# Kernel tuning notes

Hardware: AMD Instinct MI355X
Metric: run time of the kernel (lower is better)

The kernel has to match this reference:

```python
import jax, jax.numpy as jnp
import numpy as np


def setup_inputs() -> dict:
    key = jax.random.key(0)
    k1, k2 = jax.random.split(key)
    x = jax.random.normal(k1, (4, 2048, 2048), dtype=jnp.float32)
    weight = jax.random.normal(k2, (8192, 2048), dtype=jnp.float32) * 0.02
    return {"x": x, "weight": weight, "bits": 8}


def reference(x, weight, bits):
    # ---- activation quantization (per-row int8-style) ----
    scale = jnp.clip(jnp.max(jnp.abs(x), axis=-1, keepdims=True), 1e-5)  # [..., 1]
    max_val = (1 << (bits - 1)) - 1  # 127 for 8 bits
    x_q = jnp.clip(jnp.round(x * (max_val / scale)), -max_val, max_val)

    # ---- ternary weight quantization (-1, 0, 1) ----
    w_scale = jnp.mean(jnp.abs(weight))
    w_q = jnp.where(weight > 0.5 * w_scale, 1.0, 0.0) + jnp.where(
        weight < -0.5 * w_scale, -1.0, 0.0
    )

    # ---- dequantized linear: (x_q @ (w_q * w_scale)^T) / x_scale ----
    out = jnp.einsum("bsi,oi->bso", x_q, w_q * w_scale) / scale

    # ---- squared ReLU ----
    return jnp.maximum(out, 0.0) ** 2
```

## Files before the change

### kernel.cpp

```cpp
#include <hip/hip_runtime.h>
#include <hip/hip_bf16.h>

typedef __attribute__((ext_vector_type(4))) int i32x4;

#define M_DIM 8192
#define N_DIM 8192
#define K_DIM 2048
#define WCOUNT (N_DIM * K_DIM)

__global__ __launch_bounds__(256) void k_abs_partial(const float* __restrict__ w,
                                                     float* __restrict__ part) {
    int tid = blockIdx.x * 256 + threadIdx.x;
    const float4* w4 = (const float4*)w;
    float s = 0.0f;
    const int total4 = WCOUNT / 4;
    for (int i = tid; i < total4; i += 2048 * 256) {
        float4 v = w4[i];
        s += fabsf(v.x) + fabsf(v.y) + fabsf(v.z) + fabsf(v.w);
    }
    #pragma unroll
    for (int off = 1; off < 64; off <<= 1) s += __shfl_xor(s, off);
    __shared__ float red[4];
    if ((threadIdx.x & 63) == 0) red[threadIdx.x >> 6] = s;
    __syncthreads();
    if (threadIdx.x == 0)
        part[blockIdx.x] = (red[0] + red[1]) + (red[2] + red[3]);
}

__global__ __launch_bounds__(256) void k_abs_final(const float* __restrict__ part,
                                                   float* __restrict__ sum) {
    int t = threadIdx.x;
    float s = 0.0f;
    #pragma unroll
    for (int i = 0; i < 8; i++) s += part[t + i * 256];
    #pragma unroll
    for (int off = 1; off < 64; off <<= 1) s += __shfl_xor(s, off);
    __shared__ float red[4];
    if ((t & 63) == 0) red[t >> 6] = s;
    __syncthreads();
    if (t == 0) sum[0] = (red[0] + red[1]) + (red[2] + red[3]);
}

__global__ __launch_bounds__(256) void k_wquant(const float* __restrict__ w,
                                                const float* __restrict__ sum,
                                                unsigned int* __restrict__ wq) {
    const float thr = 0.5f * (sum[0] * (1.0f / 16777216.0f));
    int tid = blockIdx.x * 256 + threadIdx.x;
    const float4* w4 = (const float4*)w;
    const int total4 = WCOUNT / 4;
    for (int i = tid; i < total4; i += 2048 * 256) {
        float4 v = w4[i];
        union { signed char c[4]; unsigned int u; } q;
        q.c[0] = v.x > thr ? 1 : (v.x < -thr ? -1 : 0);
        q.c[1] = v.y > thr ? 1 : (v.y < -thr ? -1 : 0);
        q.c[2] = v.z > thr ? 1 : (v.z < -thr ? -1 : 0);
        q.c[3] = v.w > thr ? 1 : (v.w < -thr ? -1 : 0);
        wq[i] = q.u;
    }
}

__global__ __launch_bounds__(256) void k_xquant(const float* __restrict__ x,
                                                signed char* __restrict__ xq,
                                                float* __restrict__ scale) {
    const int row = blockIdx.x;
    const int t = threadIdx.x;
    const float4* xr = (const float4*)(x + (size_t)row * K_DIM);
    float4 a = xr[t * 2];
    float4 b = xr[t * 2 + 1];
    float m = fmaxf(fmaxf(fmaxf(fabsf(a.x), fabsf(a.y)), fmaxf(fabsf(a.z), fabsf(a.w))),
                    fmaxf(fmaxf(fabsf(b.x), fabsf(b.y)), fmaxf(fabsf(b.z), fabsf(b.w))));
    #pragma unroll
    for (int off = 1; off < 64; off <<= 1) m = fmaxf(m, __shfl_xor(m, off));
    __shared__ float red[4];
    if ((t & 63) == 0) red[t >> 6] = m;
    __syncthreads();
    m = fmaxf(fmaxf(red[0], red[1]), fmaxf(red[2], red[3]));
    const float sc = fmaxf(m, 1e-5f);
    if (t == 0) scale[row] = sc;
    const float r = 127.0f / sc;
    float q[8] = {a.x, a.y, a.z, a.w, b.x, b.y, b.z, b.w};
    union { signed char c[8]; uint2 v; } pk;
    #pragma unroll
    for (int j = 0; j < 8; j++) {
        float v = rintf(q[j] * r);
        v = fminf(fmaxf(v, -127.0f), 127.0f);
        pk.c[j] = (signed char)v;
    }
    *(uint2*)(xq + (size_t)row * K_DIM + t * 8) = pk.v;
}

#define GLDS16(g, l)                                                                   \
    __builtin_amdgcn_global_load_lds((const __attribute__((address_space(1))) void*)(g), \
                                     (__attribute__((address_space(3))) void*)(l), 16, 0, 0)

__global__ __launch_bounds__(256) void k_gemm(const signed char* __restrict__ Aq,
                                              const signed char* __restrict__ Bq,
                                              const float* __restrict__ scale,
                                              const float* __restrict__ sum,
                                              float* __restrict__ out) {
    __shared__ signed char As[128 * 64];
    __shared__ signed char Bs[128 * 64];

    const int t = threadIdx.x;
    const int lane = t & 63;
    const int wid = t >> 6;
    const int wr = wid >> 1;
    const int wc = wid & 1;
    const int brow = blockIdx.y;
    const int bcol = blockIdx.x;

    const int c0 = t, c1 = t + 256;
    const int g0 = ((c0 & 3) ^ ((c0 >> 3) & 3)) * 16;
    const int g1 = ((c1 & 3) ^ ((c1 >> 3) & 3)) * 16;
    const signed char* ga0 = Aq + (size_t)(brow * 128 + (c0 >> 2)) * K_DIM + g0;
    const signed char* ga1 = Aq + (size_t)(brow * 128 + (c1 >> 2)) * K_DIM + g1;
    const signed char* gb0 = Bq + (size_t)(bcol * 128 + (c0 >> 2)) * K_DIM + g0;
    const signed char* gb1 = Bq + (size_t)(bcol * 128 + (c1 >> 2)) * K_DIM + g1;
    signed char* lA0 = As + wid * 1024;
    signed char* lA1 = As + 4096 + wid * 1024;
    signed char* lB0 = Bs + wid * 1024;
    signed char* lB1 = Bs + 4096 + wid * 1024;

    i32x4 zero = {0, 0, 0, 0};
    i32x4 acc[4][4];
    #pragma unroll
    for (int m = 0; m < 4; m++)
        #pragma unroll
        for (int n = 0; n < 4; n++) acc[m][n] = zero;

    const int swz = ((lane >> 4) ^ ((lane >> 1) & 3)) * 16;
    const int a_off = (wr * 64 + (lane & 15)) * 64 + swz;
    const int b_off = (wc * 64 + (lane & 15)) * 64 + swz;

    for (int kt = 0; kt < K_DIM; kt += 64) {
        GLDS16(ga0, lA0);
        GLDS16(ga1, lA1);
        GLDS16(gb0, lB0);
        GLDS16(gb1, lB1);
        ga0 += 64; ga1 += 64; gb0 += 64; gb1 += 64;
        __syncthreads();

        i32x4 af[4], bfr[4];
        #pragma unroll
        for (int m = 0; m < 4; m++) af[m] = *(const i32x4*)&As[a_off + m * 1024];
        #pragma unroll
        for (int n = 0; n < 4; n++) bfr[n] = *(const i32x4*)&Bs[b_off + n * 1024];
        #pragma unroll
        for (int m = 0; m < 4; m++)
            #pragma unroll
            for (int n = 0; n < 4; n++)
                acc[m][n] = __builtin_amdgcn_mfma_i32_16x16x64_i8(af[m], bfr[n], acc[m][n], 0, 0, 0);
        __syncthreads();
    }

    const float wsc = sum[0] * (1.0f / 16777216.0f);
    const int rbase = brow * 128 + wr * 64 + ((lane >> 4) * 4);
    const int cbase = bcol * 128 + wc * 64 + (lane & 15);
    #pragma unroll
    for (int m = 0; m < 4; m++) {
        #pragma unroll
        for (int j = 0; j < 4; j++) {
            const int grow = rbase + m * 16 + j;
            const float coef = wsc / scale[grow];
            #pragma unroll
            for (int n = 0; n < 4; n++) {
                float v = (float)acc[m][n][j] * coef;
                v = fmaxf(v, 0.0f);
                out[(size_t)grow * N_DIM + cbase + n * 16] = v * v;
            }
        }
    }
}

extern "C" void kernel_launch(void* const* d_in, const int* in_sizes, int n_in,
                              void* d_out, int out_size, void* d_ws, size_t ws_size,
                              hipStream_t stream) {
    const float* x = (const float*)d_in[0];
    const float* w = (const float*)d_in[1];
    float* out = (float*)d_out;

    char* ws = (char*)d_ws;
    float* sum   = (float*)ws;
    float* part  = (float*)(ws + 256);
    float* scale = (float*)(ws + 16384);
    signed char* xq = (signed char*)(ws + 65536);
    signed char* wq = (signed char*)(ws + 65536 + 16777216);

    k_abs_partial<<<2048, 256, 0, stream>>>(w, part);
    k_abs_final<<<1, 256, 0, stream>>>(part, sum);
    k_wquant<<<2048, 256, 0, stream>>>(w, sum, (unsigned int*)wq);
    k_xquant<<<M_DIM, 256, 0, stream>>>(x, xq, scale);
    k_gemm<<<dim3(N_DIM / 128, M_DIM / 128), 256, 0, stream>>>(xq, wq, scale, sum, out);
}
```

Measured before the change: 223.7 us.

## Rewrite int8 GEMM with 256x256 tiles, double-buffered LDS and staged prefetch

```diff
diff --git a/kernel.cpp b/kernel.cpp
--- a/kernel.cpp
+++ b/kernel.cpp
@@ -6,6 +6,7 @@
 #define M_DIM 8192
 #define N_DIM 8192
 #define K_DIM 2048
+#define BK 128
 #define WCOUNT (N_DIM * K_DIM)
 
 __global__ __launch_bounds__(256) void k_abs_partial(const float* __restrict__ w,
@@ -93,83 +94,138 @@
     __builtin_amdgcn_global_load_lds((const __attribute__((address_space(1))) void*)(g), \
                                      (__attribute__((address_space(3))) void*)(l), 16, 0, 0)
 
-__global__ __launch_bounds__(256) void k_gemm(const signed char* __restrict__ Aq,
-                                              const signed char* __restrict__ Bq,
-                                              const float* __restrict__ scale,
-                                              const float* __restrict__ sum,
-                                              float* __restrict__ out) {
-    __shared__ signed char As[128 * 64];
-    __shared__ signed char Bs[128 * 64];
+#define AOFF(b, h) ((b) * 32768 + (h) * 16384)
+#define BOFF(b, h) (65536 + (b) * 32768 + (h) * 16384)
+#define BAR __builtin_amdgcn_s_barrier()
+#define VMCNT4 do { asm volatile("s_waitcnt vmcnt(4)" ::: "memory"); __builtin_amdgcn_sched_barrier(0); } while (0)
+#define VMCNT0 do { asm volatile("s_waitcnt vmcnt(0)" ::: "memory"); __builtin_amdgcn_sched_barrier(0); } while (0)
+
+__global__ __launch_bounds__(512, 2) void k_gemm(const signed char* __restrict__ Aq,
+                                                 const signed char* __restrict__ Bq,
+                                                 const float* __restrict__ scale,
+                                                 const float* __restrict__ sum,
+                                                 float* __restrict__ out) {
+    __shared__ signed char lds[131072];
 
     const int t = threadIdx.x;
     const int lane = t & 63;
     const int wid = t >> 6;
-    const int wr = wid >> 1;
-    const int wc = wid & 1;
-    const int brow = blockIdx.y;
-    const int bcol = blockIdx.x;
-
-    const int c0 = t, c1 = t + 256;
-    const int g0 = ((c0 & 3) ^ ((c0 >> 3) & 3)) * 16;
-    const int g1 = ((c1 & 3) ^ ((c1 >> 3) & 3)) * 16;
-    const signed char* ga0 = Aq + (size_t)(brow * 128 + (c0 >> 2)) * K_DIM + g0;
-    const signed char* ga1 = Aq + (size_t)(brow * 128 + (c1 >> 2)) * K_DIM + g1;
-    const signed char* gb0 = Bq + (size_t)(bcol * 128 + (c0 >> 2)) * K_DIM + g0;
-    const signed char* gb1 = Bq + (size_t)(bcol * 128 + (c1 >> 2)) * K_DIM + g1;
-    signed char* lA0 = As + wid * 1024;
-    signed char* lA1 = As + 4096 + wid * 1024;
-    signed char* lB0 = Bs + wid * 1024;
-    signed char* lB1 = Bs + 4096 + wid * 1024;
-
-    i32x4 zero = {0, 0, 0, 0};
-    i32x4 acc[4][4];
-    #pragma unroll
-    for (int m = 0; m < 4; m++)
+    const int wm = wid >> 2;
+    const int wn = wid & 3;
+    const int lane4 = lane & 15;
+    const int hi = lane >> 4;
+
+    const int bid = blockIdx.x;
+    const int swzb = ((bid & 7) << 7) | (bid >> 3);
+    const int brow = swzb >> 5;
+    const int bcol = swzb & 31;
+
+    const int r0 = t >> 3;
+    const int r1 = 64 + r0;
+    const int g0 = ((t & 7) ^ ((t >> 4) & 7)) << 4;
+    const int g1 = (((t + 512) & 7) ^ (((t + 512) >> 4) & 7)) << 4;
+    const int sa0 = r0 * K_DIM + g0;
+    const int sa1 = r1 * K_DIM + g1;
+    const int dst0 = wid * 1024;
+    const int dst1 = wid * 1024 + 8192;
+
+    const signed char* Abase = Aq + (size_t)(brow * 256) * K_DIM;
+    const signed char* Bbase = Bq + (size_t)(bcol * 256) * K_DIM;
+
+#define STG(gb, ldsoff, half, kt) do {                                                  \
+        GLDS16((gb) + (half) * (128 * K_DIM) + (kt) * BK + sa0, lds + (ldsoff) + dst0); \
+        GLDS16((gb) + (half) * (128 * K_DIM) + (kt) * BK + sa1, lds + (ldsoff) + dst1); \
+    } while (0)
+
+    const int swz0 = (hi ^ (lane4 >> 1)) << 4;
+    const int swz1 = ((4 + hi) ^ (lane4 >> 1)) << 4;
+    const int aB0 = AOFF(0, wm) + lane4 * 128;
+    const int aB1 = AOFF(1, wm) + lane4 * 128;
+    const int bB0 = BOFF(0, wn >> 1) + ((wn & 1) * 64 + lane4) * 128;
+    const int bB1 = BOFF(1, wn >> 1) + ((wn & 1) * 64 + lane4) * 128;
+
+    i32x4 acc[8][4];
+    #pragma unroll
+    for (int m = 0; m < 8; m++)
         #pragma unroll
-        for (int n = 0; n < 4; n++) acc[m][n] = zero;
-
-    const int swz = ((lane >> 4) ^ ((lane >> 1) & 3)) * 16;
-    const int a_off = (wr * 64 + (lane & 15)) * 64 + swz;
-    const int b_off = (wc * 64 + (lane & 15)) * 64 + swz;
-
-    for (int kt = 0; kt < K_DIM; kt += 64) {
-        GLDS16(ga0, lA0);
-        GLDS16(ga1, lA1);
-        GLDS16(gb0, lB0);
-        GLDS16(gb1, lB1);
-        ga0 += 64; ga1 += 64; gb0 += 64; gb1 += 64;
-        __syncthreads();
-
-        i32x4 af[4], bfr[4];
-        #pragma unroll
-        for (int m = 0; m < 4; m++) af[m] = *(const i32x4*)&As[a_off + m * 1024];
-        #pragma unroll
-        for (int n = 0; n < 4; n++) bfr[n] = *(const i32x4*)&Bs[b_off + n * 1024];
-        #pragma unroll
-        for (int m = 0; m < 4; m++)
-            #pragma unroll
-            for (int n = 0; n < 4; n++)
-                acc[m][n] = __builtin_amdgcn_mfma_i32_16x16x64_i8(af[m], bfr[n], acc[m][n], 0, 0, 0);
-        __syncthreads();
+        for (int n = 0; n < 4; n++) acc[m][n] = (i32x4){0, 0, 0, 0};
+    i32x4 fa0[8], fa1[8], fb0[4], fb1[4];
+
+#define RDA(base, mlo) do { _Pragma("unroll") for (int m_ = 0; m_ < 4; m_++) {          \
+        fa0[(mlo) + m_] = *(const i32x4*)&lds[(base) + ((mlo) + m_) * 2048 + swz0];     \
+        fa1[(mlo) + m_] = *(const i32x4*)&lds[(base) + ((mlo) + m_) * 2048 + swz1]; } } while (0)
+#define RDB(base, nlo) do { _Pragma("unroll") for (int n_ = 0; n_ < 2; n_++) {          \
+        fb0[(nlo) + n_] = *(const i32x4*)&lds[(base) + ((nlo) + n_) * 2048 + swz0];     \
+        fb1[(nlo) + n_] = *(const i32x4*)&lds[(base) + ((nlo) + n_) * 2048 + swz1]; } } while (0)
+#define MM(mlo, nlo) do { __builtin_amdgcn_s_setprio(1);                                \
+        _Pragma("unroll") for (int m_ = 0; m_ < 4; m_++)                                \
+        _Pragma("unroll") for (int n_ = 0; n_ < 2; n_++) {                              \
+            acc[(mlo) + m_][(nlo) + n_] = __builtin_amdgcn_mfma_i32_16x16x64_i8(        \
+                fa0[(mlo) + m_], fb0[(nlo) + n_], acc[(mlo) + m_][(nlo) + n_], 0, 0, 0);\
+            acc[(mlo) + m_][(nlo) + n_] = __builtin_amdgcn_mfma_i32_16x16x64_i8(        \
+                fa1[(mlo) + m_], fb1[(nlo) + n_], acc[(mlo) + m_][(nlo) + n_], 0, 0, 0);\
+        } __builtin_amdgcn_s_setprio(0); } while (0)
+
+    STG(Abase, AOFF(0, 0), 0, 0); STG(Abase, AOFF(0, 1), 1, 0);
+    STG(Bbase, BOFF(0, 0), 0, 0); STG(Bbase, BOFF(0, 1), 1, 0);
+    STG(Abase, AOFF(1, 0), 0, 1); STG(Abase, AOFF(1, 1), 1, 1);
+    STG(Bbase, BOFF(1, 0), 0, 1); STG(Bbase, BOFF(1, 1), 1, 1);
+    asm volatile("s_waitcnt vmcnt(8)" ::: "memory");
+    __builtin_amdgcn_sched_barrier(0);
+    BAR;
+
+    #pragma unroll 1
+    for (int i = 0; i < 8; i++) {
+        const int kt = 2 * i;
+        if (i >= 1) { STG(Bbase, BOFF(1, 0), 0, kt + 1); STG(Bbase, BOFF(1, 1), 1, kt + 1); }
+        RDA(aB0, 0); RDB(bB0, 0);
+        MM(0, 0);
+        BAR;
+        RDA(aB0, 4); RDB(bB0, 2);
+        MM(0, 2);
+        BAR;
+        MM(4, 0);
+        BAR;
+        if (i <= 6) { STG(Abase, AOFF(0, 0), 0, kt + 2); STG(Abase, AOFF(0, 1), 1, kt + 2); }
+        MM(4, 2);
+        if (i <= 6) VMCNT4; else VMCNT0;
+        BAR;
+        if (i <= 6) { STG(Bbase, BOFF(0, 0), 0, kt + 2); STG(Bbase, BOFF(0, 1), 1, kt + 2); }
+        RDA(aB1, 0); RDB(bB1, 0);
+        MM(0, 0);
+        BAR;
+        RDA(aB1, 4); RDB(bB1, 2);
+        MM(0, 2);
+        BAR;
+        MM(4, 0);
+        BAR;
+        if (i <= 6) { STG(Abase, AOFF(1, 0), 0, kt + 3); STG(Abase, AOFF(1, 1), 1, kt + 3); }
+        MM(4, 2);
+        if (i <= 6) VMCNT4; else VMCNT0;
+        BAR;
     }
 
     const float wsc = sum[0] * (1.0f / 16777216.0f);
-    const int rbase = brow * 128 + wr * 64 + ((lane >> 4) * 4);
-    const int cbase = bcol * 128 + wc * 64 + (lane & 15);
-    #pragma unroll
-    for (int m = 0; m < 4; m++) {
+    const int rb = brow * 256 + wm * 128 + hi * 4;
+    const int cb = bcol * 256 + wn * 64 + lane4;
+    #pragma unroll
+    for (int m = 0; m < 8; m++) {
         #pragma unroll
         for (int j = 0; j < 4; j++) {
-            const int grow = rbase + m * 16 + j;
+            const int grow = rb + m * 16 + j;
             const float coef = wsc / scale[grow];
             #pragma unroll
             for (int n = 0; n < 4; n++) {
                 float v = (float)acc[m][n][j] * coef;
                 v = fmaxf(v, 0.0f);
-                out[(size_t)grow * N_DIM + cbase + n * 16] = v * v;
+                out[(size_t)grow * N_DIM + cb + n * 16] = v * v;
             }
         }
     }
+#undef STG
+#undef RDA
+#undef RDB
+#undef MM
 }
 
 extern "C" void kernel_launch(void* const* d_in, const int* in_sizes, int n_in,
@@ -190,5 +246,5 @@
     k_abs_final<<<1, 256, 0, stream>>>(part, sum);
     k_wquant<<<2048, 256, 0, stream>>>(w, sum, (unsigned int*)wq);
     k_xquant<<<M_DIM, 256, 0, stream>>>(x, xq, scale);
-    k_gemm<<<dim3(N_DIM / 128, M_DIM / 128), 256, 0, stream>>>(xq, wq, scale, sum, out);
-}
+    k_gemm<<<dim3(1024), 512, 0, stream>>>(xq, wq, scale, sum, out);
+}
```

Result: faster. 202.0 us (-9.7%).

## Rewrite int8 GEMM with 256x256 tiles, 4-stage async LDS pipeline and XCD mapping

Applied to the files above, without the earlier changes.

```diff
diff --git a/kernel.cpp b/kernel.cpp
--- a/kernel.cpp
+++ b/kernel.cpp
@@ -93,83 +93,126 @@
     __builtin_amdgcn_global_load_lds((const __attribute__((address_space(1))) void*)(g), \
                                      (__attribute__((address_space(3))) void*)(l), 16, 0, 0)
 
-__global__ __launch_bounds__(256) void k_gemm(const signed char* __restrict__ Aq,
-                                              const signed char* __restrict__ Bq,
-                                              const float* __restrict__ scale,
-                                              const float* __restrict__ sum,
-                                              float* __restrict__ out) {
-    __shared__ signed char As[128 * 64];
-    __shared__ signed char Bs[128 * 64];
+#define BAR __builtin_amdgcn_s_barrier()
+#define LGKM6 do { asm volatile("s_waitcnt lgkmcnt(6)" ::: "memory"); __builtin_amdgcn_sched_barrier(0); } while (0)
+#define LGKM0 do { asm volatile("s_waitcnt lgkmcnt(0)" ::: "memory"); __builtin_amdgcn_sched_barrier(0); } while (0)
+#define VMCNT4 do { asm volatile("s_waitcnt vmcnt(4)" ::: "memory"); __builtin_amdgcn_sched_barrier(0); } while (0)
+#define VMCNT0 do { asm volatile("s_waitcnt vmcnt(0)" ::: "memory"); __builtin_amdgcn_sched_barrier(0); } while (0)
+
+__global__ __launch_bounds__(512, 2) void k_gemm(const signed char* __restrict__ Aq,
+                                                 const signed char* __restrict__ Bq,
+                                                 const float* __restrict__ scale,
+                                                 const float* __restrict__ sum,
+                                                 float* __restrict__ out) {
+    __shared__ signed char smem[131072];
 
     const int t = threadIdx.x;
     const int lane = t & 63;
     const int wid = t >> 6;
-    const int wr = wid >> 1;
-    const int wc = wid & 1;
-    const int brow = blockIdx.y;
-    const int bcol = blockIdx.x;
-
-    const int c0 = t, c1 = t + 256;
-    const int g0 = ((c0 & 3) ^ ((c0 >> 3) & 3)) * 16;
-    const int g1 = ((c1 & 3) ^ ((c1 >> 3) & 3)) * 16;
-    const signed char* ga0 = Aq + (size_t)(brow * 128 + (c0 >> 2)) * K_DIM + g0;
-    const signed char* ga1 = Aq + (size_t)(brow * 128 + (c1 >> 2)) * K_DIM + g1;
-    const signed char* gb0 = Bq + (size_t)(bcol * 128 + (c0 >> 2)) * K_DIM + g0;
-    const signed char* gb1 = Bq + (size_t)(bcol * 128 + (c1 >> 2)) * K_DIM + g1;
-    signed char* lA0 = As + wid * 1024;
-    signed char* lA1 = As + 4096 + wid * 1024;
-    signed char* lB0 = Bs + wid * 1024;
-    signed char* lB1 = Bs + 4096 + wid * 1024;
-
-    i32x4 zero = {0, 0, 0, 0};
-    i32x4 acc[4][4];
-    #pragma unroll
-    for (int m = 0; m < 4; m++)
+    const int wm = wid >> 2;
+    const int wn = wid & 3;
+    const int lane4 = lane & 15;
+    const int hi = lane >> 4;
+
+    const int bid = blockIdx.x;
+    const int xcd = bid & 7;
+    const int s_ = bid >> 3;
+    const int scol = s_ >> 4;
+    const int w_ = s_ & 15;
+    const int brow = xcd * 4 + (w_ >> 2);
+    const int bcol = scol * 4 + (w_ & 3);
+
+    const int g_ = ((t & 3) ^ ((t >> 3) & 3)) << 4;
+    const size_t sa0 = (size_t)(t >> 2) * K_DIM + g_;
+    const size_t sa1 = (size_t)(128 + (t >> 2)) * K_DIM + g_;
+    const int dst0 = wid * 1024;
+    const int dst1 = wid * 1024 + 8192;
+
+    const signed char* Abase = Aq + (size_t)(brow * 256) * K_DIM;
+    const signed char* Bbase = Bq + (size_t)(bcol * 256) * K_DIM;
+
+#define STG_A(buf, kt) do {                                                      \
+        GLDS16(Abase + (size_t)(kt) * 64 + sa0, smem + (buf) * 32768 + dst0);    \
+        GLDS16(Abase + (size_t)(kt) * 64 + sa1, smem + (buf) * 32768 + dst1); } while (0)
+#define STG_B(buf, kt) do {                                                      \
+        GLDS16(Bbase + (size_t)(kt) * 64 + sa0, smem + (buf) * 32768 + 16384 + dst0); \
+        GLDS16(Bbase + (size_t)(kt) * 64 + sa1, smem + (buf) * 32768 + 16384 + dst1); } while (0)
+
+    const int swz = (hi ^ ((lane4 >> 1) & 3)) << 4;
+    const int aRd = (wm * 128 + lane4) * 64 + swz;
+    const int bRd = 16384 + (wn * 64 + lane4) * 64 + swz;
+
+    i32x4 acc[8][4];
+    #pragma unroll
+    for (int m = 0; m < 8; m++)
         #pragma unroll
-        for (int n = 0; n < 4; n++) acc[m][n] = zero;
-
-    const int swz = ((lane >> 4) ^ ((lane >> 1) & 3)) * 16;
-    const int a_off = (wr * 64 + (lane & 15)) * 64 + swz;
-    const int b_off = (wc * 64 + (lane & 15)) * 64 + swz;
-
-    for (int kt = 0; kt < K_DIM; kt += 64) {
-        GLDS16(ga0, lA0);
-        GLDS16(ga1, lA1);
-        GLDS16(gb0, lB0);
-        GLDS16(gb1, lB1);
-        ga0 += 64; ga1 += 64; gb0 += 64; gb1 += 64;
-        __syncthreads();
-
-        i32x4 af[4], bfr[4];
-        #pragma unroll
-        for (int m = 0; m < 4; m++) af[m] = *(const i32x4*)&As[a_off + m * 1024];
-        #pragma unroll
-        for (int n = 0; n < 4; n++) bfr[n] = *(const i32x4*)&Bs[b_off + n * 1024];
-        #pragma unroll
-        for (int m = 0; m < 4; m++)
-            #pragma unroll
-            for (int n = 0; n < 4; n++)
-                acc[m][n] = __builtin_amdgcn_mfma_i32_16x16x64_i8(af[m], bfr[n], acc[m][n], 0, 0, 0);
-        __syncthreads();
-    }
+        for (int n = 0; n < 4; n++) acc[m][n] = (i32x4){0, 0, 0, 0};
+    i32x4 fa[2][8], fb[2][4];
+
+#define RD_FB(s, buf) do { _Pragma("unroll") for (int n_ = 0; n_ < 4; n_++)      \
+        fb[s][n_] = *(const i32x4*)&smem[(buf) * 32768 + bRd + n_ * 1024]; } while (0)
+#define RD_FA01(s, buf) do { _Pragma("unroll") for (int m_ = 0; m_ < 2; m_++)    \
+        fa[s][m_] = *(const i32x4*)&smem[(buf) * 32768 + aRd + m_ * 1024]; } while (0)
+#define RD_FA27(s, buf) do { _Pragma("unroll") for (int m_ = 2; m_ < 8; m_++)    \
+        fa[s][m_] = *(const i32x4*)&smem[(buf) * 32768 + aRd + m_ * 1024]; } while (0)
+#define MMQ(s, mlo) do { __builtin_amdgcn_s_setprio(1);                          \
+        _Pragma("unroll") for (int m_ = 0; m_ < 4; m_++)                         \
+        _Pragma("unroll") for (int n_ = 0; n_ < 4; n_++)                         \
+            acc[(mlo) + m_][n_] = __builtin_amdgcn_mfma_i32_16x16x64_i8(         \
+                fa[s][(mlo) + m_], fb[s][n_], acc[(mlo) + m_][n_], 0, 0, 0);     \
+        __builtin_amdgcn_s_setprio(0); __builtin_amdgcn_sched_barrier(0); } while (0)
+
+    STG_A(0, 0); STG_B(0, 0);
+    STG_A(1, 1); STG_B(1, 1);
+    STG_A(2, 2); STG_B(2, 2);
+    VMCNT4;
+    BAR;
+    RD_FB(0, 0); RD_FA01(0, 0); RD_FA27(0, 0);
+
+    #pragma unroll 1
+    for (int i = 0; i < 7; i++) {
+        const int kt = 4 * i;
+        STG_A(3, kt + 3); RD_FB(1, 1); RD_FA01(1, 1); LGKM6; MMQ(0, 0); BAR;
+        STG_B(3, kt + 3); RD_FA27(1, 1);              LGKM6; MMQ(0, 4); VMCNT4; BAR;
+        STG_A(0, kt + 4); RD_FB(0, 2); RD_FA01(0, 2); LGKM6; MMQ(1, 0); BAR;
+        STG_B(0, kt + 4); RD_FA27(0, 2);              LGKM6; MMQ(1, 4); VMCNT4; BAR;
+        STG_A(1, kt + 5); RD_FB(1, 3); RD_FA01(1, 3); LGKM6; MMQ(0, 0); BAR;
+        STG_B(1, kt + 5); RD_FA27(1, 3);              LGKM6; MMQ(0, 4); VMCNT4; BAR;
+        STG_A(2, kt + 6); RD_FB(0, 0); RD_FA01(0, 0); LGKM6; MMQ(1, 0); BAR;
+        STG_B(2, kt + 6); RD_FA27(0, 0);              LGKM6; MMQ(1, 4); VMCNT4; BAR;
+    }
+
+    STG_A(3, 31); RD_FB(1, 1); RD_FA01(1, 1); LGKM6; MMQ(0, 0); BAR;
+    STG_B(3, 31); RD_FA27(1, 1);              LGKM6; MMQ(0, 4); VMCNT4; BAR;
+    RD_FB(0, 2); RD_FA01(0, 2); LGKM6; MMQ(1, 0); BAR;
+    RD_FA27(0, 2);              LGKM6; MMQ(1, 4); VMCNT0; BAR;
+    RD_FB(1, 3); RD_FA01(1, 3); LGKM6; MMQ(0, 0); BAR;
+    RD_FA27(1, 3);              LGKM6; MMQ(0, 4); BAR;
+    LGKM0; MMQ(1, 0); MMQ(1, 4);
 
     const float wsc = sum[0] * (1.0f / 16777216.0f);
-    const int rbase = brow * 128 + wr * 64 + ((lane >> 4) * 4);
-    const int cbase = bcol * 128 + wc * 64 + (lane & 15);
-    #pragma unroll
-    for (int m = 0; m < 4; m++) {
+    const int rb = brow * 256 + wm * 128 + hi * 4;
+    const int cb = bcol * 256 + wn * 64 + lane4;
+    #pragma unroll
+    for (int m = 0; m < 8; m++) {
         #pragma unroll
         for (int j = 0; j < 4; j++) {
-            const int grow = rbase + m * 16 + j;
+            const int grow = rb + m * 16 + j;
             const float coef = wsc / scale[grow];
             #pragma unroll
             for (int n = 0; n < 4; n++) {
                 float v = (float)acc[m][n][j] * coef;
                 v = fmaxf(v, 0.0f);
-                out[(size_t)grow * N_DIM + cbase + n * 16] = v * v;
+                out[(size_t)grow * N_DIM + cb + n * 16] = v * v;
             }
         }
     }
+#undef STG_A
+#undef STG_B
+#undef RD_FB
+#undef RD_FA01
+#undef RD_FA27
+#undef MMQ
 }
 
 extern "C" void kernel_launch(void* const* d_in, const int* in_sizes, int n_in,
@@ -190,5 +233,5 @@
     k_abs_final<<<1, 256, 0, stream>>>(part, sum);
     k_wquant<<<2048, 256, 0, stream>>>(w, sum, (unsigned int*)wq);
     k_xquant<<<M_DIM, 256, 0, stream>>>(x, xq, scale);
-    k_gemm<<<dim3(N_DIM / 128, M_DIM / 128), 256, 0, stream>>>(xq, wq, scale, sum, out);
-}
+    k_gemm<<<dim3(1024), 512, 0, stream>>>(xq, wq, scale, sum, out);
+}
```

New measurement: 251.4 us. +12.4%, slower.

## Rewrite int8 GEMM with 256x256 tiles, double-buffered LDS and 32x32 MFMA

Applied to the files above, without the earlier changes.

```diff
diff --git a/kernel.cpp b/kernel.cpp
--- a/kernel.cpp
+++ b/kernel.cpp
@@ -2,10 +2,12 @@
 #include <hip/hip_bf16.h>
 
 typedef __attribute__((ext_vector_type(4))) int i32x4;
+typedef __attribute__((ext_vector_type(16))) int i32x16;
 
 #define M_DIM 8192
 #define N_DIM 8192
 #define K_DIM 2048
+#define BK 128
 #define WCOUNT (N_DIM * K_DIM)
 
 __global__ __launch_bounds__(256) void k_abs_partial(const float* __restrict__ w,
@@ -93,83 +95,139 @@
     __builtin_amdgcn_global_load_lds((const __attribute__((address_space(1))) void*)(g), \
                                      (__attribute__((address_space(3))) void*)(l), 16, 0, 0)
 
-__global__ __launch_bounds__(256) void k_gemm(const signed char* __restrict__ Aq,
-                                              const signed char* __restrict__ Bq,
-                                              const float* __restrict__ scale,
-                                              const float* __restrict__ sum,
-                                              float* __restrict__ out) {
-    __shared__ signed char As[128 * 64];
-    __shared__ signed char Bs[128 * 64];
+#define AOFF(b, h) ((b) * 32768 + (h) * 16384)
+#define BOFF(b, h) (65536 + (b) * 32768 + (h) * 16384)
+#define SYNC do { asm volatile("s_waitcnt vmcnt(0) lgkmcnt(0)" ::: "memory");          \
+        __builtin_amdgcn_sched_barrier(0); __builtin_amdgcn_s_barrier(); } while (0)
+
+__global__ __launch_bounds__(512, 2) void k_gemm(const signed char* __restrict__ Aq,
+                                                 const signed char* __restrict__ Bq,
+                                                 const float* __restrict__ scale,
+                                                 const float* __restrict__ sum,
+                                                 float* __restrict__ out) {
+    __shared__ signed char lds[131072];
 
     const int t = threadIdx.x;
     const int lane = t & 63;
     const int wid = t >> 6;
-    const int wr = wid >> 1;
-    const int wc = wid & 1;
-    const int brow = blockIdx.y;
-    const int bcol = blockIdx.x;
-
-    const int c0 = t, c1 = t + 256;
-    const int g0 = ((c0 & 3) ^ ((c0 >> 3) & 3)) * 16;
-    const int g1 = ((c1 & 3) ^ ((c1 >> 3) & 3)) * 16;
-    const signed char* ga0 = Aq + (size_t)(brow * 128 + (c0 >> 2)) * K_DIM + g0;
-    const signed char* ga1 = Aq + (size_t)(brow * 128 + (c1 >> 2)) * K_DIM + g1;
-    const signed char* gb0 = Bq + (size_t)(bcol * 128 + (c0 >> 2)) * K_DIM + g0;
-    const signed char* gb1 = Bq + (size_t)(bcol * 128 + (c1 >> 2)) * K_DIM + g1;
-    signed char* lA0 = As + wid * 1024;
-    signed char* lA1 = As + 4096 + wid * 1024;
-    signed char* lB0 = Bs + wid * 1024;
-    signed char* lB1 = Bs + 4096 + wid * 1024;
-
-    i32x4 zero = {0, 0, 0, 0};
-    i32x4 acc[4][4];
+    const int wm = wid >> 2;
+    const int wn = wid & 3;
+    const int l31 = lane & 31;
+    const int kg = lane >> 5;
+
+    const int bid = blockIdx.x;
+    const int xcd = bid & 7;
+    const int s_ = bid >> 3;
+    const int scol = s_ >> 4;
+    const int w_ = s_ & 15;
+    const int brow = xcd * 4 + (w_ >> 2);
+    const int bcol = scol * 4 + (w_ & 3);
+
+    const int g_ = ((t & 7) ^ ((t >> 4) & 7)) << 4;
+    const size_t sa0 = (size_t)(t >> 3) * K_DIM + g_;
+    const size_t sa1 = (size_t)(64 + (t >> 3)) * K_DIM + g_;
+    const int dst0 = wid * 1024;
+    const int dst1 = wid * 1024 + 8192;
+
+    const signed char* Abase = Aq + (size_t)(brow * 256) * K_DIM;
+    const signed char* Bbase = Bq + (size_t)(bcol * 256) * K_DIM;
+
+#define STGH(gb, lo) do { GLDS16((gb) + sa0, lds + (lo) + dst0);                  \
+                          GLDS16((gb) + sa1, lds + (lo) + dst1); } while (0)
+#define STG_A(buf, kt) do { STGH(Abase + (size_t)(kt) * BK, AOFF(buf, 0));        \
+        STGH(Abase + 128 * (size_t)K_DIM + (size_t)(kt) * BK, AOFF(buf, 1)); } while (0)
+#define STG_B(buf, kt) do { STGH(Bbase + (size_t)(kt) * BK, BOFF(buf, 0));        \
+        STGH(Bbase + 128 * (size_t)K_DIM + (size_t)(kt) * BK, BOFF(buf, 1)); } while (0)
+
+    const int rswz = (l31 >> 1) & 7;
+    const int ko0 = ((0 * 2 + kg) ^ rswz) << 4;
+    const int ko1 = ((1 * 2 + kg) ^ rswz) << 4;
+    const int ko2 = ((2 * 2 + kg) ^ rswz) << 4;
+    const int ko3 = ((3 * 2 + kg) ^ rswz) << 4;
+    const int aB0 = AOFF(0, wm) + l31 * 128;
+    const int aB1 = AOFF(1, wm) + l31 * 128;
+    const int bB0 = BOFF(0, wn >> 1) + ((wn & 1) * 64 + l31) * 128;
+    const int bB1 = BOFF(1, wn >> 1) + ((wn & 1) * 64 + l31) * 128;
+
+    i32x16 acc[4][2];
     #pragma unroll
     for (int m = 0; m < 4; m++)
         #pragma unroll
-        for (int n = 0; n < 4; n++) acc[m][n] = zero;
-
-    const int swz = ((lane >> 4) ^ ((lane >> 1) & 3)) * 16;
-    const int a_off = (wr * 64 + (lane & 15)) * 64 + swz;
-    const int b_off = (wc * 64 + (lane & 15)) * 64 + swz;
-
-    for (int kt = 0; kt < K_DIM; kt += 64) {
-        GLDS16(ga0, lA0);
-        GLDS16(ga1, lA1);
-        GLDS16(gb0, lB0);
-        GLDS16(gb1, lB1);
-        ga0 += 64; ga1 += 64; gb0 += 64; gb1 += 64;
-        __syncthreads();
-
-        i32x4 af[4], bfr[4];
-        #pragma unroll
-        for (int m = 0; m < 4; m++) af[m] = *(const i32x4*)&As[a_off + m * 1024];
-        #pragma unroll
-        for (int n = 0; n < 4; n++) bfr[n] = *(const i32x4*)&Bs[b_off + n * 1024];
-        #pragma unroll
-        for (int m = 0; m < 4; m++)
-            #pragma unroll
-            for (int n = 0; n < 4; n++)
-                acc[m][n] = __builtin_amdgcn_mfma_i32_16x16x64_i8(af[m], bfr[n], acc[m][n], 0, 0, 0);
-        __syncthreads();
+        for (int n = 0; n < 2; n++)
+            acc[m][n] = (i32x16){0,0,0,0,0,0,0,0,0,0,0,0,0,0,0,0};
+    i32x4 fA0[4], fB0[2], fA1[4], fB1[2];
+
+#define RDS(FA, FB, ab, bb, ko) do {                                              \
+        _Pragma("unroll") for (int m_ = 0; m_ < 4; m_++)                          \
+            FA[m_] = *(const i32x4*)&lds[(ab) + m_ * 4096 + (ko)];                \
+        _Pragma("unroll") for (int n_ = 0; n_ < 2; n_++)                          \
+            FB[n_] = *(const i32x4*)&lds[(bb) + n_ * 4096 + (ko)]; } while (0)
+#define MMX(FA, FB) do { __builtin_amdgcn_s_setprio(1);                           \
+        _Pragma("unroll") for (int m_ = 0; m_ < 4; m_++)                          \
+        _Pragma("unroll") for (int n_ = 0; n_ < 2; n_++)                          \
+            acc[m_][n_] = __builtin_amdgcn_mfma_i32_32x32x32_i8(                  \
+                FA[m_], FB[n_], acc[m_][n_], 0, 0, 0);                            \
+        __builtin_amdgcn_s_setprio(0); } while (0)
+
+    STG_B(0, 0);
+    STG_A(0, 0);
+    STG_B(1, 1);
+    asm volatile("s_waitcnt vmcnt(4)" ::: "memory");
+    __builtin_amdgcn_sched_barrier(0);
+    __builtin_amdgcn_s_barrier();
+    RDS(fA0, fB0, aB0, bB0, ko0);
+
+    #pragma unroll 1
+    for (int i = 0; i < 8; i++) {
+        const int kt = 2 * i;
+        STG_A(1, kt + 1);
+        RDS(fA1, fB1, aB0, bB0, ko1);
+        MMX(fA0, fB0);
+        RDS(fA0, fB0, aB0, bB0, ko2);
+        MMX(fA1, fB1);
+        RDS(fA1, fB1, aB0, bB0, ko3);
+        MMX(fA0, fB0);
+        SYNC;
+        if (i < 7) STG_B(0, kt + 2);
+        RDS(fA0, fB0, aB1, bB1, ko0);
+        MMX(fA1, fB1);
+        if (i < 7) STG_A(0, kt + 2);
+        RDS(fA1, fB1, aB1, bB1, ko1);
+        MMX(fA0, fB0);
+        RDS(fA0, fB0, aB1, bB1, ko2);
+        MMX(fA1, fB1);
+        RDS(fA1, fB1, aB1, bB1, ko3);
+        MMX(fA0, fB0);
+        SYNC;
+        if (i < 7) {
+            STG_B(1, kt + 3);
+            RDS(fA0, fB0, aB0, bB0, ko0);
+        }
+        MMX(fA1, fB1);
     }
 
     const float wsc = sum[0] * (1.0f / 16777216.0f);
-    const int rbase = brow * 128 + wr * 64 + ((lane >> 4) * 4);
-    const int cbase = bcol * 128 + wc * 64 + (lane & 15);
+    const int rb = brow * 256 + wm * 128 + 4 * kg;
+    const int cb = bcol * 256 + wn * 64 + l31;
     #pragma unroll
     for (int m = 0; m < 4; m++) {
         #pragma unroll
-        for (int j = 0; j < 4; j++) {
-            const int grow = rbase + m * 16 + j;
+        for (int r = 0; r < 16; r++) {
+            const int grow = rb + m * 32 + (r & 3) + 8 * (r >> 2);
             const float coef = wsc / scale[grow];
             #pragma unroll
-            for (int n = 0; n < 4; n++) {
-                float v = (float)acc[m][n][j] * coef;
+            for (int n = 0; n < 2; n++) {
+                float v = (float)acc[m][n][r] * coef;
                 v = fmaxf(v, 0.0f);
-                out[(size_t)grow * N_DIM + cbase + n * 16] = v * v;
+                out[(size_t)grow * N_DIM + cb + n * 32] = v * v;
             }
         }
     }
+#undef STGH
+#undef STG_A
+#undef STG_B
+#undef RDS
+#undef MMX
 }
 
 extern "C" void kernel_launch(void* const* d_in, const int* in_sizes, int n_in,
@@ -190,5 +248,5 @@
     k_abs_final<<<1, 256, 0, stream>>>(part, sum);
     k_wquant<<<2048, 256, 0, stream>>>(w, sum, (unsigned int*)wq);
     k_xquant<<<M_DIM, 256, 0, stream>>>(x, xq, scale);
-    k_gemm<<<dim3(N_DIM / 128, M_DIM / 128), 256, 0, stream>>>(xq, wq, scale, sum, out);
-}
+    k_gemm<<<dim3(1024), 512, 0, stream>>>(xq, wq, scale, sum, out);
+}
```

Result: faster. 198.6 us (-11.2%).
